# Kernel tuning notes

Hardware: AMD Instinct MI355X
Metric: run time of the kernel (lower is better)

The kernel has to match this reference:

```python
import jax, jax.numpy as jnp
import numpy as np

B, T, I, H = 64, 512, 1024, 1024


def setup_inputs() -> dict:
    key = jax.random.key(0)
    k1, k2, k3, k4 = jax.random.split(key, 4)
    s_in = 1.0 / np.sqrt(I)
    s_h = 1.0 / np.sqrt(H)
    return {
        "x": jax.random.normal(k1, (B, T, I), dtype=jnp.float32),
        "Wih": jax.random.normal(k2, (4 * H, I), dtype=jnp.float32) * s_in,
        "Whh": jax.random.normal(k3, (4 * H, H), dtype=jnp.float32) * s_h,
        "b": jax.random.normal(k4, (4 * H,), dtype=jnp.float32) * s_h,
    }


def reference(x, Wih, Whh, b):
    """Sequential RNN layer (LSTM cell step) over (batch, seq_len, input).

    Mirrors RNNLayer.forward_tensor: zero-initialized state, per-timestep
    step(), stacked outputs plus final state. The Python time loop is
    expressed as a single lax.scan (one fused launch).
    """
    batch = x.shape[0]
    h0 = jnp.zeros((batch, H), dtype=x.dtype)
    c0 = jnp.zeros((batch, H), dtype=x.dtype)

    def step(carry, xt):  # xt: [B, I]
        h, c = carry
        gates = xt @ Wih.T + h @ Whh.T + b  # [B, 4H]
        i_g, f_g, g_g, o_g = jnp.split(gates, 4, axis=-1)
        c_new = jax.nn.sigmoid(f_g) * c + jax.nn.sigmoid(i_g) * jnp.tanh(g_g)
        h_new = jax.nn.sigmoid(o_g) * jnp.tanh(c_new)
        return (h_new, c_new), h_new

    xs = jnp.swapaxes(x, 0, 1)  # [T, B, I] for scan over time
    (h_T, c_T), outs = jax.lax.scan(step, (h0, c0), xs)
    outputs = jnp.swapaxes(outs, 0, 1)  # [B, T, H]
    return outputs, (h_T, c_T)
```

## Files before the change

### kernel.cpp

```cpp
#include <hip/hip_runtime.h>
#include <stdint.h>


typedef __bf16 bf16x8 __attribute__((ext_vector_type(8)));
typedef float f32x4 __attribute__((ext_vector_type(4)));

#define BATCH 64
#define TSEQ 512
#define HID 1024
#define MROWS (BATCH * TSEQ)
#define NGATE 4096

__device__ __forceinline__ unsigned short f2bf(float f) {
  union { float f; unsigned u; } v; v.f = f;
  unsigned r = (v.u + 0x7FFFu + ((v.u >> 16) & 1u)) >> 16;
  return (unsigned short)r;
}
__device__ __forceinline__ float bf2f(unsigned short u) {
  union { unsigned u; float f; } v; v.u = ((unsigned)u) << 16;
  return v.f;
}

__global__ void cvt_kernel(const float* __restrict__ src,
                           unsigned short* __restrict__ dst, int n4) {
  int i = blockIdx.x * blockDim.x + threadIdx.x;
  const int stride = gridDim.x * blockDim.x;
  for (; i < n4; i += stride) {
    float4 f = ((const float4*)src)[i];
    ushort4 u;
    u.x = f2bf(f.x); u.y = f2bf(f.y); u.z = f2bf(f.z); u.w = f2bf(f.w);
    ((ushort4*)dst)[i] = u;
  }
}

__device__ __forceinline__ void gl_lds16(const unsigned short* g, unsigned short* lds) {
  __builtin_amdgcn_global_load_lds(
      (const __attribute__((address_space(1))) unsigned int*)g,
      (__attribute__((address_space(3))) unsigned int*)lds, 16, 0, 0);
}

__global__ __launch_bounds__(256, 2) void gemm_xg(
    const unsigned short* __restrict__ A,
    const unsigned short* __restrict__ B,
    const float* __restrict__ bias,
    unsigned short* __restrict__ Xg)
{
  __shared__ __align__(16) unsigned short Asm[128 * 32];
  __shared__ __align__(16) unsigned short Bsm[128 * 32];
  const int tid = threadIdx.x;
  const int lane = tid & 63;
  const int wave = tid >> 6;
  const int row0 = blockIdx.y * 128;
  const int col0 = blockIdx.x * 128;
  const int wm = (wave >> 1) * 64;
  const int wn = (wave & 1) * 64;
  const int s_ml = lane >> 2;
  const int s_q = ((lane & 3) ^ (s_ml >> 1)) & 3;
  const int fm = lane & 15;
  const int fq = lane >> 4;
  const int swz = ((fq ^ (fm >> 1)) & 3) * 8;

  f32x4 acc[4][4] = {};

  for (int kt = 0; kt < 32; ++kt) {
    const int k0 = kt * 32;
    __syncthreads();
#pragma unroll
    for (int gI = 0; gI < 2; ++gI) {
      const int grp = wave * 2 + gI;
      const unsigned short* ga =
          A + (size_t)(row0 + grp * 16 + s_ml) * 1024 + k0 + s_q * 8;
      gl_lds16(ga, &Asm[grp * 512]);
      const unsigned short* gb =
          B + (size_t)(col0 + grp * 16 + s_ml) * 1024 + k0 + s_q * 8;
      gl_lds16(gb, &Bsm[grp * 512]);
    }
    __syncthreads();
    bf16x8 af[4], bfv[4];
#pragma unroll
    for (int mt = 0; mt < 4; ++mt) {
      const int m = wm + mt * 16 + fm;
      af[mt] = *(const bf16x8*)&Asm[(m >> 4) * 512 + fm * 32 + swz];
    }
#pragma unroll
    for (int nt = 0; nt < 4; ++nt) {
      const int n = wn + nt * 16 + fm;
      bfv[nt] = *(const bf16x8*)&Bsm[(n >> 4) * 512 + fm * 32 + swz];
    }
#pragma unroll
    for (int mt = 0; mt < 4; ++mt)
#pragma unroll
      for (int nt = 0; nt < 4; ++nt)
        acc[mt][nt] = __builtin_amdgcn_mfma_f32_16x16x32_bf16(
            af[mt], bfv[nt], acc[mt][nt], 0, 0, 0);
  }
#pragma unroll
  for (int nt = 0; nt < 4; ++nt) {
    const int nb = col0 + wn + nt * 16;
    const int pbase = ((nb & 1023) >> 4) * 64 + (nb >> 10) * 16;
    const float bv = bias[nb + fm];
#pragma unroll
    for (int mt = 0; mt < 4; ++mt) {
#pragma unroll
      for (int r = 0; r < 4; ++r) {
        const int row = row0 + wm + mt * 16 + fq * 4 + r;
        Xg[(size_t)row * 4096 + pbase + fm] = f2bf(acc[mt][nt][r] + bv);
      }
    }
  }
}

__device__ __forceinline__ bf16x8 load_h16B(const unsigned short* p) {
  union { unsigned long long q[2]; bf16x8 v; } u;
  const unsigned long long* q = (const unsigned long long*)p;
  u.q[0] = __hip_atomic_load(q, __ATOMIC_RELAXED, __HIP_MEMORY_SCOPE_AGENT);
  u.q[1] = __hip_atomic_load(q + 1, __ATOMIC_RELAXED, __HIP_MEMORY_SCOPE_AGENT);
  return u.v;
}

__global__ __launch_bounds__(256, 1) void lstm_seq(
    const unsigned short* __restrict__ Whh,
    const unsigned short* __restrict__ Xg,
    float* __restrict__ out,
    unsigned short* __restrict__ hbuf,
    unsigned int* __restrict__ flags)
{
  __shared__ float part[4][16][68];
  const int tid = threadIdx.x;
  const int lane = tid & 63;
  const int wave = tid >> 6;
  const int bn = blockIdx.x >> 2;
  const int mi = blockIdx.x & 3;
  const int fm = lane & 15;
  const int fq = lane >> 4;
  unsigned int* flg = flags + mi * 64 * 32;
  unsigned int* myflag = flg + bn * 32;
  unsigned int* pollp = flg + (wave * 16 + (lane & 15)) * 32;

  bf16x8 bfrag[4][8];
#pragma unroll
  for (int g = 0; g < 4; ++g) {
    const unsigned short* wrow =
        Whh + (size_t)(g * 1024 + bn * 16 + fm) * 1024 + wave * 256 + fq * 8;
#pragma unroll
    for (int ki = 0; ki < 8; ++ki) bfrag[g][ki] = *(const bf16x8*)(wrow + ki * 32);
  }

  const int em = tid >> 4, ej = tid & 15;
  const int gb = mi * 16 + em;
  const int gj = bn * 16 + ej;
  float c_reg = 0.f;

  unsigned short* h0 = hbuf;
  unsigned short* h1 = hbuf + BATCH * HID;

  const unsigned short* xrow = Xg + (size_t)gb * TSEQ * 4096 + bn * 64;
  float xpre[4];
#pragma unroll
  for (int g = 0; g < 4; ++g) xpre[g] = bf2f(xrow[g * 16 + ej]);

  for (int t = 0; t < TSEQ; ++t) {
    const unsigned short* hp = (t & 1) ? h1 : h0;
    unsigned short* hn = (t & 1) ? h0 : h1;
    const unsigned short* ab =
        hp + (size_t)(mi * 16 + fm) * 1024 + wave * 256 + fq * 8;

    float xcur[4];
#pragma unroll
    for (int g = 0; g < 4; ++g) xcur[g] = xpre[g];
    if (t < TSEQ - 1) {
      const unsigned short* xn = xrow + (size_t)(t + 1) * 4096;
#pragma unroll
      for (int g = 0; g < 4; ++g) xpre[g] = bf2f(xn[g * 16 + ej]);
    }

    if (t > 0) {
      for (;;) {
        const unsigned f = __hip_atomic_load(pollp, __ATOMIC_RELAXED,
                                             __HIP_MEMORY_SCOPE_AGENT);
        if (__all((int)(f >= (unsigned)t))) break;
        __builtin_amdgcn_s_sleep(1);
      }
      __builtin_amdgcn_sched_barrier(0);
    }

    bf16x8 afr[8];
#pragma unroll
    for (int ki = 0; ki < 8; ++ki) afr[ki] = load_h16B(ab + ki * 32);

    f32x4 acc[4] = {};
#pragma unroll
    for (int ki = 0; ki < 8; ++ki)
#pragma unroll
      for (int g = 0; g < 4; ++g)
        acc[g] = __builtin_amdgcn_mfma_f32_16x16x32_bf16(afr[ki], bfrag[g][ki],
                                                         acc[g], 0, 0, 0);

#pragma unroll
    for (int g = 0; g < 4; ++g)
#pragma unroll
      for (int r = 0; r < 4; ++r)
        part[wave][fq * 4 + r][g * 16 + fm] = acc[g][r];
    __syncthreads();

    float gate[4];
#pragma unroll
    for (int g = 0; g < 4; ++g) {
      float s = part[0][em][g * 16 + ej] + part[1][em][g * 16 + ej] +
                part[2][em][g * 16 + ej] + part[3][em][g * 16 + ej];
      gate[g] = s + xcur[g];
    }
    const float ig = 1.f / (1.f + __expf(-gate[0]));
    const float fg = 1.f / (1.f + __expf(-gate[1]));
    const float gg = 1.f - 2.f / (__expf(2.f * gate[2]) + 1.f);
    const float og = 1.f / (1.f + __expf(-gate[3]));
    c_reg = fg * c_reg + ig * gg;
    const float th = 1.f - 2.f / (__expf(2.f * c_reg) + 1.f);
    const float hv = og * th;

    __hip_atomic_store(&hn[(size_t)gb * HID + gj], f2bf(hv),
                       __ATOMIC_RELAXED, __HIP_MEMORY_SCOPE_AGENT);

    if (t == TSEQ - 1) {
      out[((size_t)gb * TSEQ + t) * HID + gj] = hv;
      out[(size_t)BATCH * TSEQ * HID + (size_t)gb * HID + gj] = hv;
      out[(size_t)BATCH * TSEQ * HID + (size_t)BATCH * HID + (size_t)gb * HID + gj] = c_reg;
      break;
    }

    __syncthreads();
    if (tid == 0)
      __hip_atomic_store(myflag, (unsigned)(t + 1),
                         __ATOMIC_RELAXED, __HIP_MEMORY_SCOPE_AGENT);

    out[((size_t)gb * TSEQ + t) * HID + gj] = hv;
  }
}

extern "C" void kernel_launch(void* const* d_in, const int* in_sizes, int n_in,
                              void* d_out, int out_size, void* d_ws, size_t ws_size,
                              hipStream_t stream) {
  (void)in_sizes; (void)n_in; (void)out_size;
  const float* x   = (const float*)d_in[0];
  const float* Wih = (const float*)d_in[1];
  const float* Whh = (const float*)d_in[2];
  const float* b   = (const float*)d_in[3];
  float* out = (float*)d_out;

  char* ws = (char*)d_ws;
  unsigned short* hbuf   = (unsigned short*)(ws + 1024);
  unsigned short* x_bf   = (unsigned short*)(ws + 263168);
  unsigned short* wih_bf = (unsigned short*)(ws + 263168 + 67108864);
  unsigned short* whh_bf = (unsigned short*)(ws + 263168 + 75497472);
  unsigned short* xg     = (unsigned short*)(ws + 263168 + 83886080);
  unsigned int* flags = (unsigned int*)x_bf;
  const size_t needed = 263168ULL + 83886080ULL + 268435456ULL;
  if (ws_size < needed) return;

  hipMemsetAsync(hbuf, 0, 2 * BATCH * HID * sizeof(unsigned short), stream);

  cvt_kernel<<<2048, 256, 0, stream>>>(x, x_bf, (MROWS * 1024) / 4);
  cvt_kernel<<<512, 256, 0, stream>>>(Wih, wih_bf, (NGATE * 1024) / 4);
  cvt_kernel<<<512, 256, 0, stream>>>(Whh, whh_bf, (NGATE * 1024) / 4);

  dim3 g(32, 256);
  gemm_xg<<<g, 256, 0, stream>>>(x_bf, wih_bf, b, xg);

  hipMemsetAsync(flags, 0, 4 * 64 * 128, stream);

  lstm_seq<<<256, 256, 0, stream>>>(whh_bf, xg, out, hbuf, flags);
}
```

Baseline: 2.235 ms.

## Replace per-block flag polling with step-tagged hidden state words

Each hidden value is now stored as a 32-bit word that packs the bf16 value with the timestep, so consumers poll the data itself until every tag matches. This removes the separate flag array, the second __syncthreads and the flag store per step, and the shared partial-sum buffer is double-buffered to avoid a write-after-read hazard. The cost is twice the bytes per hidden-state read, repeated polling traffic on the full operand, and repacking of the words into bf16 fragments.

```diff
diff --git a/kernel.cpp b/kernel.cpp
--- a/kernel.cpp
+++ b/kernel.cpp
@@ -110,22 +110,13 @@
   }
 }
 
-__device__ __forceinline__ bf16x8 load_h16B(const unsigned short* p) {
-  union { unsigned long long q[2]; bf16x8 v; } u;
-  const unsigned long long* q = (const unsigned long long*)p;
-  u.q[0] = __hip_atomic_load(q, __ATOMIC_RELAXED, __HIP_MEMORY_SCOPE_AGENT);
-  u.q[1] = __hip_atomic_load(q + 1, __ATOMIC_RELAXED, __HIP_MEMORY_SCOPE_AGENT);
-  return u.v;
-}
-
 __global__ __launch_bounds__(256, 1) void lstm_seq(
     const unsigned short* __restrict__ Whh,
     const unsigned short* __restrict__ Xg,
     float* __restrict__ out,
-    unsigned short* __restrict__ hbuf,
-    unsigned int* __restrict__ flags)
+    unsigned int* __restrict__ htag)
 {
-  __shared__ float part[4][16][68];
+  __shared__ float part[2][4][16][68];
   const int tid = threadIdx.x;
   const int lane = tid & 63;
   const int wave = tid >> 6;
@@ -133,9 +124,6 @@
   const int mi = blockIdx.x & 3;
   const int fm = lane & 15;
   const int fq = lane >> 4;
-  unsigned int* flg = flags + mi * 64 * 32;
-  unsigned int* myflag = flg + bn * 32;
-  unsigned int* pollp = flg + (wave * 16 + (lane & 15)) * 32;
 
   bf16x8 bfrag[4][8];
 #pragma unroll
@@ -151,8 +139,7 @@
   const int gj = bn * 16 + ej;
   float c_reg = 0.f;
 
-  unsigned short* h0 = hbuf;
-  unsigned short* h1 = hbuf + BATCH * HID;
+  const size_t b64 = ((size_t)(mi * 16 + fm) * HID + wave * 256 + fq * 8) >> 1;
 
   const unsigned short* xrow = Xg + (size_t)gb * TSEQ * 4096 + bn * 64;
   float xpre[4];
@@ -160,10 +147,9 @@
   for (int g = 0; g < 4; ++g) xpre[g] = bf2f(xrow[g * 16 + ej]);
 
   for (int t = 0; t < TSEQ; ++t) {
-    const unsigned short* hp = (t & 1) ? h1 : h0;
-    unsigned short* hn = (t & 1) ? h0 : h1;
-    const unsigned short* ab =
-        hp + (size_t)(mi * 16 + fm) * 1024 + wave * 256 + fq * 8;
+    const unsigned texp = (unsigned)t & 0xffffu;
+    const unsigned long long* hb =
+        (const unsigned long long*)(htag + (size_t)(t & 1) * BATCH * HID) + b64;
 
     float xcur[4];
 #pragma unroll
@@ -174,19 +160,39 @@
       for (int g = 0; g < 4; ++g) xpre[g] = bf2f(xn[g * 16 + ej]);
     }
 
-    if (t > 0) {
-      for (;;) {
-        const unsigned f = __hip_atomic_load(pollp, __ATOMIC_RELAXED,
-                                             __HIP_MEMORY_SCOPE_AGENT);
-        if (__all((int)(f >= (unsigned)t))) break;
-        __builtin_amdgcn_s_sleep(1);
+    unsigned long long q[8][4];
+    for (;;) {
+      unsigned orq = 0u;
+#pragma unroll
+      for (int ki = 0; ki < 8; ++ki)
+#pragma unroll
+        for (int j = 0; j < 4; ++j)
+          q[ki][j] = __hip_atomic_load(hb + ki * 16 + j, __ATOMIC_RELAXED,
+                                       __HIP_MEMORY_SCOPE_AGENT);
+#pragma unroll
+      for (int ki = 0; ki < 8; ++ki)
+#pragma unroll
+        for (int j = 0; j < 4; ++j) {
+          const unsigned lo = (unsigned)q[ki][j];
+          const unsigned hi = (unsigned)(q[ki][j] >> 32);
+          orq |= (lo ^ texp) | (hi ^ texp);
+        }
+      if (__all((int)((orq & 0xffffu) == 0u))) break;
+      __builtin_amdgcn_s_sleep(1);
+    }
+
+    bf16x8 afr[8];
+#pragma unroll
+    for (int ki = 0; ki < 8; ++ki) {
+      union { unsigned u[4]; bf16x8 v; } pk;
+#pragma unroll
+      for (int j = 0; j < 4; ++j) {
+        const unsigned lo = (unsigned)q[ki][j];
+        const unsigned hi = (unsigned)(q[ki][j] >> 32);
+        pk.u[j] = (lo >> 16) | (hi & 0xffff0000u);
       }
-      __builtin_amdgcn_sched_barrier(0);
-    }
-
-    bf16x8 afr[8];
-#pragma unroll
-    for (int ki = 0; ki < 8; ++ki) afr[ki] = load_h16B(ab + ki * 32);
+      afr[ki] = pk.v;
+    }
 
     f32x4 acc[4] = {};
 #pragma unroll
@@ -196,18 +202,19 @@
         acc[g] = __builtin_amdgcn_mfma_f32_16x16x32_bf16(afr[ki], bfrag[g][ki],
                                                          acc[g], 0, 0, 0);
 
+    float (*pp)[16][68] = part[t & 1];
 #pragma unroll
     for (int g = 0; g < 4; ++g)
 #pragma unroll
       for (int r = 0; r < 4; ++r)
-        part[wave][fq * 4 + r][g * 16 + fm] = acc[g][r];
+        pp[wave][fq * 4 + r][g * 16 + fm] = acc[g][r];
     __syncthreads();
 
     float gate[4];
 #pragma unroll
     for (int g = 0; g < 4; ++g) {
-      float s = part[0][em][g * 16 + ej] + part[1][em][g * 16 + ej] +
-                part[2][em][g * 16 + ej] + part[3][em][g * 16 + ej];
+      float s = pp[0][em][g * 16 + ej] + pp[1][em][g * 16 + ej] +
+                pp[2][em][g * 16 + ej] + pp[3][em][g * 16 + ej];
       gate[g] = s + xcur[g];
     }
     const float ig = 1.f / (1.f + __expf(-gate[0]));
@@ -218,22 +225,16 @@
     const float th = 1.f - 2.f / (__expf(2.f * c_reg) + 1.f);
     const float hv = og * th;
 
-    __hip_atomic_store(&hn[(size_t)gb * HID + gj], f2bf(hv),
-                       __ATOMIC_RELAXED, __HIP_MEMORY_SCOPE_AGENT);
-
-    if (t == TSEQ - 1) {
+    if (t < TSEQ - 1) {
+      const unsigned tagged = ((unsigned)f2bf(hv) << 16) | ((unsigned)(t + 1) & 0xffffu);
+      __hip_atomic_store(&htag[(size_t)((t + 1) & 1) * BATCH * HID + (size_t)gb * HID + gj],
+                         tagged, __ATOMIC_RELAXED, __HIP_MEMORY_SCOPE_AGENT);
+      out[((size_t)gb * TSEQ + t) * HID + gj] = hv;
+    } else {
       out[((size_t)gb * TSEQ + t) * HID + gj] = hv;
       out[(size_t)BATCH * TSEQ * HID + (size_t)gb * HID + gj] = hv;
       out[(size_t)BATCH * TSEQ * HID + (size_t)BATCH * HID + (size_t)gb * HID + gj] = c_reg;
-      break;
-    }
-
-    __syncthreads();
-    if (tid == 0)
-      __hip_atomic_store(myflag, (unsigned)(t + 1),
-                         __ATOMIC_RELAXED, __HIP_MEMORY_SCOPE_AGENT);
-
-    out[((size_t)gb * TSEQ + t) * HID + gj] = hv;
+    }
   }
 }
 
@@ -248,16 +249,13 @@
   float* out = (float*)d_out;
 
   char* ws = (char*)d_ws;
-  unsigned short* hbuf   = (unsigned short*)(ws + 1024);
   unsigned short* x_bf   = (unsigned short*)(ws + 263168);
   unsigned short* wih_bf = (unsigned short*)(ws + 263168 + 67108864);
   unsigned short* whh_bf = (unsigned short*)(ws + 263168 + 75497472);
   unsigned short* xg     = (unsigned short*)(ws + 263168 + 83886080);
-  unsigned int* flags = (unsigned int*)x_bf;
+  unsigned int* htag = (unsigned int*)x_bf;
   const size_t needed = 263168ULL + 83886080ULL + 268435456ULL;
   if (ws_size < needed) return;
-
-  hipMemsetAsync(hbuf, 0, 2 * BATCH * HID * sizeof(unsigned short), stream);
 
   cvt_kernel<<<2048, 256, 0, stream>>>(x, x_bf, (MROWS * 1024) / 4);
   cvt_kernel<<<512, 256, 0, stream>>>(Wih, wih_bf, (NGATE * 1024) / 4);
@@ -266,7 +264,7 @@
   dim3 g(32, 256);
   gemm_xg<<<g, 256, 0, stream>>>(x_bf, wih_bf, b, xg);
 
-  hipMemsetAsync(flags, 0, 4 * 64 * 128, stream);
-
-  lstm_seq<<<256, 256, 0, stream>>>(whh_bf, xg, out, hbuf, flags);
-}
+  hipMemsetAsync(htag, 0, 2 * BATCH * HID * sizeof(unsigned int), stream);
+
+  lstm_seq<<<256, 256, 0, stream>>>(whh_bf, xg, out, htag);
+}
```

Result: slower. 3.928 ms (+75.7%).

## Halve persistent LSTM blocks by giving each block 32 hidden units

Applied to the files above, without the earlier changes.

The persistent recurrent kernel now runs 128 blocks instead of 256, and each block owns 32 hidden columns across all four gates. Each block keeps twice as many Whh fragments in registers and issues 8 MFMA tiles per k-step, and each thread computes two cell outputs. The aim is to cut the number of blocks taking part in the per-timestep flag barrier and polling, which lowers synchronisation cost on the serial critical path. The trade-offs are double the MFMA work per block per step, higher register pressure (64 bf16x8 fragments), and fewer active CUs.

```diff
diff --git a/kernel.cpp b/kernel.cpp
--- a/kernel.cpp
+++ b/kernel.cpp
@@ -125,7 +125,7 @@
     unsigned short* __restrict__ hbuf,
     unsigned int* __restrict__ flags)
 {
-  __shared__ float part[4][16][68];
+  __shared__ float part[4][16][132];
   const int tid = threadIdx.x;
   const int lane = tid & 63;
   const int wave = tid >> 6;
@@ -133,31 +133,42 @@
   const int mi = blockIdx.x & 3;
   const int fm = lane & 15;
   const int fq = lane >> 4;
-  unsigned int* flg = flags + mi * 64 * 32;
+  unsigned int* flg = flags + mi * 32 * 32;
   unsigned int* myflag = flg + bn * 32;
-  unsigned int* pollp = flg + (wave * 16 + (lane & 15)) * 32;
-
-  bf16x8 bfrag[4][8];
-#pragma unroll
-  for (int g = 0; g < 4; ++g) {
-    const unsigned short* wrow =
-        Whh + (size_t)(g * 1024 + bn * 16 + fm) * 1024 + wave * 256 + fq * 8;
-#pragma unroll
-    for (int ki = 0; ki < 8; ++ki) bfrag[g][ki] = *(const bf16x8*)(wrow + ki * 32);
-  }
-
-  const int em = tid >> 4, ej = tid & 15;
+  unsigned int* pollp = flg + (wave * 8 + (lane & 7)) * 32;
+
+  bf16x8 bfrag[8][8];
+#pragma unroll
+  for (int g = 0; g < 4; ++g)
+#pragma unroll
+    for (int u = 0; u < 2; ++u) {
+      const unsigned short* wrow =
+          Whh + (size_t)(g * 1024 + bn * 32 + u * 16 + fm) * 1024 + wave * 256 + fq * 8;
+#pragma unroll
+      for (int ki = 0; ki < 8; ++ki)
+        bfrag[g * 2 + u][ki] = *(const bf16x8*)(wrow + ki * 32);
+    }
+
+  const int em = tid >> 4;
+  const int tl = tid & 15;
+  const int c0 = 2 * tl, c1 = 2 * tl + 1;
+  const int lo0 = c0 & 15, hi0 = c0 >> 4;
+  const int lo1 = c1 & 15, hi1 = c1 >> 4;
   const int gb = mi * 16 + em;
-  const int gj = bn * 16 + ej;
-  float c_reg = 0.f;
+  const int gj0 = bn * 32 + c0;
+  const int gj1 = bn * 32 + c1;
+  float c_reg0 = 0.f, c_reg1 = 0.f;
 
   unsigned short* h0 = hbuf;
   unsigned short* h1 = hbuf + BATCH * HID;
 
-  const unsigned short* xrow = Xg + (size_t)gb * TSEQ * 4096 + bn * 64;
-  float xpre[4];
-#pragma unroll
-  for (int g = 0; g < 4; ++g) xpre[g] = bf2f(xrow[g * 16 + ej]);
+  const unsigned short* xrow = Xg + (size_t)gb * TSEQ * 4096 + bn * 128;
+  float xpre0[4], xpre1[4];
+#pragma unroll
+  for (int g = 0; g < 4; ++g) {
+    xpre0[g] = bf2f(xrow[hi0 * 64 + g * 16 + lo0]);
+    xpre1[g] = bf2f(xrow[hi1 * 64 + g * 16 + lo1]);
+  }
 
   for (int t = 0; t < TSEQ; ++t) {
     const unsigned short* hp = (t & 1) ? h1 : h0;
@@ -165,13 +176,16 @@
     const unsigned short* ab =
         hp + (size_t)(mi * 16 + fm) * 1024 + wave * 256 + fq * 8;
 
-    float xcur[4];
-#pragma unroll
-    for (int g = 0; g < 4; ++g) xcur[g] = xpre[g];
+    float xcur0[4], xcur1[4];
+#pragma unroll
+    for (int g = 0; g < 4; ++g) { xcur0[g] = xpre0[g]; xcur1[g] = xpre1[g]; }
     if (t < TSEQ - 1) {
       const unsigned short* xn = xrow + (size_t)(t + 1) * 4096;
 #pragma unroll
-      for (int g = 0; g < 4; ++g) xpre[g] = bf2f(xn[g * 16 + ej]);
+      for (int g = 0; g < 4; ++g) {
+        xpre0[g] = bf2f(xn[hi0 * 64 + g * 16 + lo0]);
+        xpre1[g] = bf2f(xn[hi1 * 64 + g * 16 + lo1]);
+      }
     }
 
     if (t > 0) {
@@ -188,43 +202,62 @@
 #pragma unroll
     for (int ki = 0; ki < 8; ++ki) afr[ki] = load_h16B(ab + ki * 32);
 
-    f32x4 acc[4] = {};
+    f32x4 acc[8] = {};
 #pragma unroll
     for (int ki = 0; ki < 8; ++ki)
 #pragma unroll
-      for (int g = 0; g < 4; ++g)
-        acc[g] = __builtin_amdgcn_mfma_f32_16x16x32_bf16(afr[ki], bfrag[g][ki],
-                                                         acc[g], 0, 0, 0);
-
-#pragma unroll
-    for (int g = 0; g < 4; ++g)
+      for (int nt = 0; nt < 8; ++nt)
+        acc[nt] = __builtin_amdgcn_mfma_f32_16x16x32_bf16(afr[ki], bfrag[nt][ki],
+                                                          acc[nt], 0, 0, 0);
+
+#pragma unroll
+    for (int nt = 0; nt < 8; ++nt)
 #pragma unroll
       for (int r = 0; r < 4; ++r)
-        part[wave][fq * 4 + r][g * 16 + fm] = acc[g][r];
+        part[wave][fq * 4 + r][nt * 16 + fm] = acc[nt][r];
     __syncthreads();
 
-    float gate[4];
+    float gate0[4], gate1[4];
 #pragma unroll
     for (int g = 0; g < 4; ++g) {
-      float s = part[0][em][g * 16 + ej] + part[1][em][g * 16 + ej] +
-                part[2][em][g * 16 + ej] + part[3][em][g * 16 + ej];
-      gate[g] = s + xcur[g];
-    }
-    const float ig = 1.f / (1.f + __expf(-gate[0]));
-    const float fg = 1.f / (1.f + __expf(-gate[1]));
-    const float gg = 1.f - 2.f / (__expf(2.f * gate[2]) + 1.f);
-    const float og = 1.f / (1.f + __expf(-gate[3]));
-    c_reg = fg * c_reg + ig * gg;
-    const float th = 1.f - 2.f / (__expf(2.f * c_reg) + 1.f);
-    const float hv = og * th;
-
-    __hip_atomic_store(&hn[(size_t)gb * HID + gj], f2bf(hv),
+      const int ci0 = (g * 2 + hi0) * 16 + lo0;
+      const int ci1 = (g * 2 + hi1) * 16 + lo1;
+      gate0[g] = part[0][em][ci0] + part[1][em][ci0] +
+                 part[2][em][ci0] + part[3][em][ci0] + xcur0[g];
+      gate1[g] = part[0][em][ci1] + part[1][em][ci1] +
+                 part[2][em][ci1] + part[3][em][ci1] + xcur1[g];
+    }
+    const float ig0 = 1.f / (1.f + __expf(-gate0[0]));
+    const float fg0 = 1.f / (1.f + __expf(-gate0[1]));
+    const float gg0 = 1.f - 2.f / (__expf(2.f * gate0[2]) + 1.f);
+    const float og0 = 1.f / (1.f + __expf(-gate0[3]));
+    c_reg0 = fg0 * c_reg0 + ig0 * gg0;
+    const float th0 = 1.f - 2.f / (__expf(2.f * c_reg0) + 1.f);
+    const float hv0 = og0 * th0;
+
+    const float ig1 = 1.f / (1.f + __expf(-gate1[0]));
+    const float fg1 = 1.f / (1.f + __expf(-gate1[1]));
+    const float gg1 = 1.f - 2.f / (__expf(2.f * gate1[2]) + 1.f);
+    const float og1 = 1.f / (1.f + __expf(-gate1[3]));
+    c_reg1 = fg1 * c_reg1 + ig1 * gg1;
+    const float th1 = 1.f - 2.f / (__expf(2.f * c_reg1) + 1.f);
+    const float hv1 = og1 * th1;
+
+    __hip_atomic_store(&hn[(size_t)gb * HID + gj0], f2bf(hv0),
                        __ATOMIC_RELAXED, __HIP_MEMORY_SCOPE_AGENT);
+    __hip_atomic_store(&hn[(size_t)gb * HID + gj1], f2bf(hv1),
+                       __ATOMIC_RELAXED, __HIP_MEMORY_SCOPE_AGENT);
 
     if (t == TSEQ - 1) {
-      out[((size_t)gb * TSEQ + t) * HID + gj] = hv;
-      out[(size_t)BATCH * TSEQ * HID + (size_t)gb * HID + gj] = hv;
-      out[(size_t)BATCH * TSEQ * HID + (size_t)BATCH * HID + (size_t)gb * HID + gj] = c_reg;
+      const size_t ob = (size_t)gb * TSEQ + t;
+      out[ob * HID + gj0] = hv0;
+      out[ob * HID + gj1] = hv1;
+      const size_t hT = (size_t)BATCH * TSEQ * HID + (size_t)gb * HID;
+      out[hT + gj0] = hv0;
+      out[hT + gj1] = hv1;
+      const size_t cT = hT + (size_t)BATCH * HID;
+      out[cT + gj0] = c_reg0;
+      out[cT + gj1] = c_reg1;
       break;
     }
 
@@ -233,7 +266,8 @@
       __hip_atomic_store(myflag, (unsigned)(t + 1),
                          __ATOMIC_RELAXED, __HIP_MEMORY_SCOPE_AGENT);
 
-    out[((size_t)gb * TSEQ + t) * HID + gj] = hv;
+    out[((size_t)gb * TSEQ + t) * HID + gj0] = hv0;
+    out[((size_t)gb * TSEQ + t) * HID + gj1] = hv1;
   }
 }
 
@@ -266,7 +300,7 @@
   dim3 g(32, 256);
   gemm_xg<<<g, 256, 0, stream>>>(x_bf, wih_bf, b, xg);
 
-  hipMemsetAsync(flags, 0, 4 * 64 * 128, stream);
-
-  lstm_seq<<<256, 256, 0, stream>>>(whh_bf, xg, out, hbuf, flags);
-}
+  hipMemsetAsync(flags, 0, 4 * 32 * 128, stream);
+
+  lstm_seq<<<128, 256, 0, stream>>>(whh_bf, xg, out, hbuf, flags);
+}
```

Measured after the change: 2.738 ms. 1.22x slower.

## Give each wave full K for its own hidden units, removing block barriers

Applied to the files above, without the earlier changes.

Each wave now owns 4 hidden units across all four gates and runs the full K=1024 reduction itself, so cross-wave partial sums in shared memory and both __syncthreads per timestep go away. Wave-local LDS handles the transpose into the elementwise layout, and a shared atomic counter lets the last wave to finish publish the block's progress flag. Each wave now holds 32 weight fragments and loads 32 h fragments per step, which raises register pressure and per-wave latency on the recurrent critical path.

```diff
diff --git a/kernel.cpp b/kernel.cpp
--- a/kernel.cpp
+++ b/kernel.cpp
@@ -125,7 +125,8 @@
     unsigned short* __restrict__ hbuf,
     unsigned int* __restrict__ flags)
 {
-  __shared__ float part[4][16][68];
+  __shared__ float xpose[4][16][20];
+  __shared__ unsigned cnt;
   const int tid = threadIdx.x;
   const int lane = tid & 63;
   const int wave = tid >> 6;
@@ -135,35 +136,38 @@
   const int fq = lane >> 4;
   unsigned int* flg = flags + mi * 64 * 32;
   unsigned int* myflag = flg + bn * 32;
-  unsigned int* pollp = flg + (wave * 16 + (lane & 15)) * 32;
-
-  bf16x8 bfrag[4][8];
-#pragma unroll
-  for (int g = 0; g < 4; ++g) {
+  unsigned int* pollp = flg + lane * 32;
+
+  if (tid == 0) cnt = 0;
+  __syncthreads();
+
+  bf16x8 bfrag[32];
+  {
+    const int g = fm >> 2, u = fm & 3;
     const unsigned short* wrow =
-        Whh + (size_t)(g * 1024 + bn * 16 + fm) * 1024 + wave * 256 + fq * 8;
-#pragma unroll
-    for (int ki = 0; ki < 8; ++ki) bfrag[g][ki] = *(const bf16x8*)(wrow + ki * 32);
-  }
-
-  const int em = tid >> 4, ej = tid & 15;
-  const int gb = mi * 16 + em;
-  const int gj = bn * 16 + ej;
+        Whh + (size_t)(g * 1024 + bn * 16 + wave * 4 + u) * 1024 + fq * 8;
+#pragma unroll
+    for (int ki = 0; ki < 32; ++ki) bfrag[ki] = *(const bf16x8*)(wrow + ki * 32);
+  }
+
+  const int row_e = lane >> 2, u_e = lane & 3;
+  const int gb = mi * 16 + row_e;
+  const int gj = bn * 16 + wave * 4 + u_e;
   float c_reg = 0.f;
 
   unsigned short* h0 = hbuf;
   unsigned short* h1 = hbuf + BATCH * HID;
 
-  const unsigned short* xrow = Xg + (size_t)gb * TSEQ * 4096 + bn * 64;
+  const unsigned short* xrow =
+      Xg + (size_t)gb * TSEQ * 4096 + bn * 64 + wave * 4 + u_e;
   float xpre[4];
 #pragma unroll
-  for (int g = 0; g < 4; ++g) xpre[g] = bf2f(xrow[g * 16 + ej]);
+  for (int g = 0; g < 4; ++g) xpre[g] = bf2f(xrow[g * 16]);
 
   for (int t = 0; t < TSEQ; ++t) {
     const unsigned short* hp = (t & 1) ? h1 : h0;
     unsigned short* hn = (t & 1) ? h0 : h1;
-    const unsigned short* ab =
-        hp + (size_t)(mi * 16 + fm) * 1024 + wave * 256 + fq * 8;
+    const unsigned short* ab = hp + (size_t)(mi * 16 + fm) * 1024 + fq * 8;
 
     float xcur[4];
 #pragma unroll
@@ -171,7 +175,7 @@
     if (t < TSEQ - 1) {
       const unsigned short* xn = xrow + (size_t)(t + 1) * 4096;
 #pragma unroll
-      for (int g = 0; g < 4; ++g) xpre[g] = bf2f(xn[g * 16 + ej]);
+      for (int g = 0; g < 4; ++g) xpre[g] = bf2f(xn[g * 16]);
     }
 
     if (t > 0) {
@@ -184,32 +188,27 @@
       __builtin_amdgcn_sched_barrier(0);
     }
 
-    bf16x8 afr[8];
-#pragma unroll
-    for (int ki = 0; ki < 8; ++ki) afr[ki] = load_h16B(ab + ki * 32);
+    bf16x8 afr[32];
+#pragma unroll
+    for (int ki = 0; ki < 32; ++ki) afr[ki] = load_h16B(ab + ki * 32);
 
     f32x4 acc[4] = {};
 #pragma unroll
-    for (int ki = 0; ki < 8; ++ki)
-#pragma unroll
-      for (int g = 0; g < 4; ++g)
-        acc[g] = __builtin_amdgcn_mfma_f32_16x16x32_bf16(afr[ki], bfrag[g][ki],
-                                                         acc[g], 0, 0, 0);
-
+    for (int ki = 0; ki < 32; ++ki)
+      acc[ki & 3] = __builtin_amdgcn_mfma_f32_16x16x32_bf16(
+          afr[ki], bfrag[ki], acc[ki & 3], 0, 0, 0);
+    const f32x4 accs = (acc[0] + acc[1]) + (acc[2] + acc[3]);
+
+#pragma unroll
+    for (int r = 0; r < 4; ++r) xpose[wave][fq * 4 + r][fm] = accs[r];
+    asm volatile("s_waitcnt lgkmcnt(0)" ::: "memory");
+    __builtin_amdgcn_sched_barrier(0);
+
+    float gate[4];
 #pragma unroll
     for (int g = 0; g < 4; ++g)
-#pragma unroll
-      for (int r = 0; r < 4; ++r)
-        part[wave][fq * 4 + r][g * 16 + fm] = acc[g][r];
-    __syncthreads();
-
-    float gate[4];
-#pragma unroll
-    for (int g = 0; g < 4; ++g) {
-      float s = part[0][em][g * 16 + ej] + part[1][em][g * 16 + ej] +
-                part[2][em][g * 16 + ej] + part[3][em][g * 16 + ej];
-      gate[g] = s + xcur[g];
-    }
+      gate[g] = xpose[wave][row_e][g * 4 + u_e] + xcur[g];
+
     const float ig = 1.f / (1.f + __expf(-gate[0]));
     const float fg = 1.f / (1.f + __expf(-gate[1]));
     const float gg = 1.f - 2.f / (__expf(2.f * gate[2]) + 1.f);
@@ -228,10 +227,14 @@
       break;
     }
 
-    __syncthreads();
-    if (tid == 0)
-      __hip_atomic_store(myflag, (unsigned)(t + 1),
-                         __ATOMIC_RELAXED, __HIP_MEMORY_SCOPE_AGENT);
+    asm volatile("s_waitcnt vmcnt(0)" ::: "memory");
+    __builtin_amdgcn_sched_barrier(0);
+    if (lane == 0) {
+      const unsigned old = atomicAdd(&cnt, 1u);
+      if (old == 4u * (unsigned)t + 3u)
+        __hip_atomic_store(myflag, (unsigned)(t + 1),
+                           __ATOMIC_RELAXED, __HIP_MEMORY_SCOPE_AGENT);
+    }
 
     out[((size_t)gb * TSEQ + t) * HID + gj] = hv;
   }
```

Result: slower. 5.496 ms (+145.9%).
